# Performance work log

Measured on AMD Instinct MI355X. Metric: run time of the kernel, lower is better.

## Reference

```python
import jax, jax.numpy as jnp
import numpy as np

SAMPLING_FACTOR = 5


def setup_inputs() -> dict:
    key = jax.random.key(0)
    kq, kk, kv, ki = jax.random.split(key, 4)
    B, L, D = 32, 2048, 64
    return {
        "query_states": jax.random.normal(kq, (B, L, D), dtype=jnp.float32),
        "key_states": jax.random.normal(kk, (B, L, D), dtype=jnp.float32),
        "value_states": jax.random.normal(kv, (B, L, D), dtype=jnp.float32),
        "index_sample": jax.random.randint(ki, (L,), 0, L, dtype=jnp.int32),
    }


def reference(query_states, key_states, value_states, index_sample):
    B, L_Q, d_k = query_states.shape
    L_K = key_states.shape[1]
    log_L_K = int(np.ceil(np.log1p(L_K)))
    log_L_Q = int(np.ceil(np.log1p(L_Q)))
    U_part = min(SAMPLING_FACTOR * L_Q * log_L_K, L_K)
    u = min(SAMPLING_FACTOR * log_L_Q, L_Q)

    # random key sampling (indices supplied deterministically)
    idx = index_sample[:U_part]                       # [U_part]
    K_sample = jnp.take(key_states, idx, axis=1)      # [B, U_part, d]

    # sparsity measurement M(q) = max_k q.k - mean (original divides by L_K)
    Q_K_sample = jnp.einsum("bqd,bkd->bqk", query_states, K_sample)  # [B, L_Q, U_part]
    M = jnp.max(Q_K_sample, axis=-1) - jnp.sum(Q_K_sample, axis=-1) / jnp.float32(L_K)

    # top-u query selection
    _, M_top = jax.lax.top_k(M, u)                    # [B, u]
    Q_reduce = jnp.take_along_axis(query_states, M_top[..., None], axis=1)  # [B, u, d]

    # reduced attention
    attn_scores = jnp.einsum("bud,bkd->buk", Q_reduce, key_states) / jnp.sqrt(jnp.float32(d_k))
    attn_probs = jax.nn.softmax(attn_scores, axis=-1)
    attn_output = jnp.einsum("buk,bkd->bud", attn_probs, value_states)
    return attn_output, attn_scores
```

## Files before the change

### kernel.cpp

```cpp
#include <hip/hip_runtime.h>
#include <math.h>

#define BB 32
#define LL 2048
#define DD 64
#define UU 40
#define CC 64
#define FSEG 16
#define PSTR 42
#define NEG_BIG (-3.0e38f)

typedef __attribute__((ext_vector_type(8))) short short8;
typedef __attribute__((ext_vector_type(4))) float f32x4;
typedef unsigned long long ull;
typedef unsigned int uint;
typedef unsigned short ushort_t;

__device__ __forceinline__ unsigned short f2bf(float f) {
  uint u = __float_as_uint(f);
  u += 0x7FFFu + ((u >> 16) & 1u);
  return (unsigned short)(u >> 16);
}
__device__ __forceinline__ uint fsort(float f) {
  uint u = __float_as_uint(f);
  return (u & 0x80000000u) ? ~u : (u | 0x80000000u);
}
__device__ __forceinline__ ull shfl_xor_u64(ull x, int m) {
  uint lo = (uint)x, hi = (uint)(x >> 32);
  lo = __shfl_xor(lo, m);
  hi = __shfl_xor(hi, m);
  return ((ull)hi << 32) | lo;
}
__device__ __forceinline__ int4 pack_bf16x8(float4 a, float4 c4) {
  int4 o;
  o.x = (int)(f2bf(a.x) | ((uint)f2bf(a.y) << 16));
  o.y = (int)(f2bf(a.z) | ((uint)f2bf(a.w) << 16));
  o.z = (int)(f2bf(c4.x) | ((uint)f2bf(c4.y) << 16));
  o.w = (int)(f2bf(c4.z) | ((uint)f2bf(c4.w) << 16));
  return o;
}

__global__ __launch_bounds__(256) void prep_ksum_kernel(const float* __restrict__ K,
                                                        const int* __restrict__ idx,
                                                        ushort_t* __restrict__ Kg,
                                                        float* __restrict__ Kpart) {
  int p = blockIdx.x, b = blockIdx.y, t = threadIdx.x;
  int g = t & 7;
  float4 sa = {0.f, 0.f, 0.f, 0.f}, sb = {0.f, 0.f, 0.f, 0.f};
#pragma unroll
  for (int it = 0; it < 4; ++it) {
    int r = p * 128 + it * 32 + (t >> 3);
    int gk = idx[r];
    const float* src = K + ((size_t)b * LL + gk) * DD + g * 8;
    float4 a = *(const float4*)src;
    float4 c4 = *(const float4*)(src + 4);
    sa.x += a.x; sa.y += a.y; sa.z += a.z; sa.w += a.w;
    sb.x += c4.x; sb.y += c4.y; sb.z += c4.z; sb.w += c4.w;
    *(int4*)(Kg + ((size_t)b * LL + r) * DD + g * 8) = pack_bf16x8(a, c4);
  }
  __shared__ float red[32][64];
  int rt = t >> 3;
  *(float4*)&red[rt][g * 8] = sa;
  *(float4*)&red[rt][g * 8 + 4] = sb;
  __syncthreads();
  if (t < 64) {
    float s = 0.f;
#pragma unroll
    for (int r = 0; r < 32; ++r) s += red[r][t];
    Kpart[(b * 16 + p) * 64 + t] = s;
  }
}

__global__ __launch_bounds__(256) void mfma_m_kernel(const float* __restrict__ Q,
                                                     const ushort_t* __restrict__ Kg,
                                                     const float* __restrict__ Kpart,
                                                     float* __restrict__ Mb) {
  __shared__ __align__(16) ushort_t Qs[128 * 64];
  __shared__ __align__(16) ushort_t Ks[128 * 64];
  __shared__ float Mmax[2][128];
  __shared__ float KsumS[64];

  int b = blockIdx.y, q0 = blockIdx.x * 128;
  int t = threadIdx.x;
  int w = t >> 6, L = t & 63;

  if (t < 64) {
    float s = 0.f;
#pragma unroll
    for (int p = 0; p < 16; ++p) s += Kpart[(b * 16 + p) * 64 + t];
    KsumS[t] = s;
  }

  {
    int g = t & 7;
#pragma unroll
    for (int it = 0; it < 4; ++it) {
      int r = it * 32 + (t >> 3);
      const float* src = Q + ((size_t)b * LL + q0 + r) * DD + g * 8;
      float4 a = *(const float4*)src;
      float4 c4 = *(const float4*)(src + 4);
      *(int4*)&Qs[r * 64 + 8 * (g ^ (r & 7))] = pack_bf16x8(a, c4);
    }
  }

  f32x4 mx[4];
#pragma unroll
  for (int i = 0; i < 4; ++i) mx[i] = (f32x4){NEG_BIG, NEG_BIG, NEG_BIG, NEG_BIG};

  const int waveQ = 64 * (w & 1);
  const int waveK = 64 * (w >> 1);
  const int lm = L & 15;
  const int lq = L >> 4;

  for (int c = 0; c < LL / 128; ++c) {
    __syncthreads();
    {
      int g = t & 7;
#pragma unroll
      for (int it = 0; it < 4; ++it) {
        int r = it * 32 + (t >> 3);
        int4 v = *(const int4*)(Kg + ((size_t)b * LL + c * 128 + r) * DD + g * 8);
        *(int4*)&Ks[r * 64 + 8 * (g ^ (r & 7))] = v;
      }
    }
    __syncthreads();

    f32x4 acc[4][4];
#pragma unroll
    for (int i = 0; i < 4; ++i)
#pragma unroll
      for (int j = 0; j < 4; ++j) acc[i][j] = (f32x4){0.f, 0.f, 0.f, 0.f};

#pragma unroll
    for (int s = 0; s < 2; ++s) {
      int g = 4 * s + lq;
      short8 A[4];
#pragma unroll
      for (int qt = 0; qt < 4; ++qt) {
        int r = waveQ + 16 * qt + lm;
        A[qt] = *(const short8*)&Qs[r * 64 + 8 * (g ^ (r & 7))];
      }
#pragma unroll
      for (int kt = 0; kt < 4; ++kt) {
        int rB = waveK + 16 * kt + lm;
        short8 Bf = *(const short8*)&Ks[rB * 64 + 8 * (g ^ (rB & 7))];
#pragma unroll
        for (int qt = 0; qt < 4; ++qt) {
          acc[qt][kt] = __builtin_amdgcn_mfma_f32_16x16x32_bf16(A[qt], Bf, acc[qt][kt], 0, 0, 0);
        }
      }
    }
#pragma unroll
    for (int qt = 0; qt < 4; ++qt)
#pragma unroll
      for (int kt = 0; kt < 4; ++kt) {
#pragma unroll
        for (int r4 = 0; r4 < 4; ++r4) mx[qt][r4] = fmaxf(mx[qt][r4], acc[qt][kt][r4]);
      }
  }

#pragma unroll
  for (int qt = 0; qt < 4; ++qt) {
#pragma unroll
    for (int r4 = 0; r4 < 4; ++r4) {
      float v = mx[qt][r4];
      v = fmaxf(v, __shfl_xor(v, 1));
      v = fmaxf(v, __shfl_xor(v, 2));
      v = fmaxf(v, __shfl_xor(v, 4));
      v = fmaxf(v, __shfl_xor(v, 8));
      mx[qt][r4] = v;
    }
  }
  if (lm < 4) {
    int qt = lm;
#pragma unroll
    for (int r4 = 0; r4 < 4; ++r4) {
      Mmax[w >> 1][waveQ + 16 * qt + 4 * lq + r4] = mx[qt][r4];
    }
  }
  __syncthreads();

  if (t < 128) {
    float m = fmaxf(Mmax[0][t], Mmax[1][t]);
    const float4* Qr = (const float4*)(Q + ((size_t)b * LL + q0 + t) * DD);
    float s = 0.f;
#pragma unroll
    for (int i = 0; i < 16; ++i) {
      float4 qv = Qr[i];
      s += qv.x * KsumS[4 * i] + qv.y * KsumS[4 * i + 1] + qv.z * KsumS[4 * i + 2] +
           qv.w * KsumS[4 * i + 3];
    }
    Mb[b * LL + q0 + t] = m - s * (1.0f / (float)LL);
  }
}

__global__ __launch_bounds__(256) void cand_kernel(const float* __restrict__ Mb,
                                                   int* __restrict__ cand) {
  int b = blockIdx.x, t = threadIdx.x;
  int w = t >> 6;
  float v[8];
#pragma unroll
  for (int i = 0; i < 8; ++i) v[i] = Mb[b * LL + t + 256 * i];
  __shared__ ull warr[4];
  __shared__ ull winls;
  for (int round = 0; round < CC; ++round) {
    float bv = v[0];
    int bi = 0;
#pragma unroll
    for (int i = 1; i < 8; ++i)
      if (v[i] > bv) { bv = v[i]; bi = i; }
    ull key = ((ull)fsort(bv) << 32) | (ull)(uint)(t + 256 * bi);
#pragma unroll
    for (int m = 1; m < 64; m <<= 1) {
      ull o = shfl_xor_u64(key, m);
      if (o > key) key = o;
    }
    if ((t & 63) == 0) warr[w] = key;
    __syncthreads();
    if (t == 0) {
      ull k = warr[0];
#pragma unroll
      for (int i = 1; i < 4; ++i)
        if (warr[i] > k) k = warr[i];
      winls = k;
      cand[b * CC + round] = (int)(k & 0xFFFFFFFFull);
    }
    __syncthreads();
    int wj = (int)(winls & 0xFFFFFFFFull);
    if (t == (wj & 255)) v[wj >> 8] = NEG_BIG;
  }
}

__global__ __launch_bounds__(256) void rescue_kernel(const float* __restrict__ Q,
                                                     const float* __restrict__ K,
                                                     const int* __restrict__ idx,
                                                     const int* __restrict__ cand,
                                                     float* __restrict__ Mpart) {
  __shared__ float Qc[64][68];
  __shared__ float Kt[128][68];
  __shared__ float red[64][33];
  __shared__ int cidx[CC];
  int seg = blockIdx.x, b = blockIdx.y, t = threadIdx.x;

  if (t < CC) cidx[t] = cand[b * CC + t];
  __syncthreads();
  for (int li = t; li < 64 * 16; li += 256) {
    int row = li >> 4, g4 = li & 15;
    *(float4*)&Qc[row][4 * g4] =
        *(const float4*)(Q + ((size_t)b * LL + cidx[row]) * DD + 4 * g4);
  }
  for (int li = t; li < 128 * 16; li += 256) {
    int row = li >> 4, g4 = li & 15;
    int gk = idx[seg * 128 + row];
    *(float4*)&Kt[row][4 * g4] =
        *(const float4*)(K + ((size_t)b * LL + gk) * DD + 4 * g4);
  }
  __syncthreads();

  int tx = t & 7;
  int ty = t >> 3;
  float acc[8][4];
#pragma unroll
  for (int i = 0; i < 8; ++i)
#pragma unroll
    for (int j = 0; j < 4; ++j) acc[i][j] = 0.f;

#pragma unroll 4
  for (int dd = 0; dd < 64; dd += 4) {
    float4 qf[8];
#pragma unroll
    for (int i = 0; i < 8; ++i) qf[i] = *(const float4*)&Qc[tx + 8 * i][dd];
    float4 kf[4];
#pragma unroll
    for (int j = 0; j < 4; ++j) kf[j] = *(const float4*)&Kt[ty + 32 * j][dd];
#pragma unroll
    for (int i = 0; i < 8; ++i)
#pragma unroll
      for (int j = 0; j < 4; ++j) {
        float d = acc[i][j];
        d = fmaf(qf[i].x, kf[j].x, d);
        d = fmaf(qf[i].y, kf[j].y, d);
        d = fmaf(qf[i].z, kf[j].z, d);
        d = fmaf(qf[i].w, kf[j].w, d);
        acc[i][j] = d;
      }
  }

#pragma unroll
  for (int i = 0; i < 8; ++i) {
    float m = fmaxf(fmaxf(acc[i][0], acc[i][1]), fmaxf(acc[i][2], acc[i][3]));
    red[tx + 8 * i][ty] = m;
  }
  __syncthreads();
  if (t < CC) {
    float m = red[t][0];
#pragma unroll
    for (int tt = 1; tt < 32; ++tt) m = fmaxf(m, red[t][tt]);
    Mpart[((size_t)b * CC + t) * FSEG + seg] = m;
  }
}

__global__ __launch_bounds__(64) void select_kernel(const float* __restrict__ Q,
                                                    const float* __restrict__ Kpart,
                                                    const int* __restrict__ cand,
                                                    const float* __restrict__ Mpart,
                                                    int* __restrict__ topi) {
  int b = blockIdx.x, t = threadIdx.x;
  __shared__ float KsumS[64];
  __shared__ ull keys[CC];
  {
    float s = 0.f;
#pragma unroll
    for (int p = 0; p < 16; ++p) s += Kpart[(b * 16 + p) * 64 + t];
    KsumS[t] = s;
  }
  __syncthreads();
  int ci = cand[b * CC + t];
  float m = NEG_BIG;
#pragma unroll
  for (int s = 0; s < FSEG; ++s) m = fmaxf(m, Mpart[((size_t)b * CC + t) * FSEG + s]);
  const float4* Qr = (const float4*)(Q + ((size_t)b * LL + ci) * DD);
  float s = 0.f;
#pragma unroll
  for (int i = 0; i < 16; ++i) {
    float4 qv = Qr[i];
    s += qv.x * KsumS[4 * i] + qv.y * KsumS[4 * i + 1] + qv.z * KsumS[4 * i + 2] +
         qv.w * KsumS[4 * i + 3];
  }
  float Mf = m - s * (1.0f / (float)LL);
  ull key = ((ull)fsort(Mf) << 32) | (ull)(uint)(2047 - ci);
  keys[t] = key;
  __syncthreads();
  int rank = 0;
#pragma unroll 8
  for (int j = 0; j < CC; ++j) rank += (keys[j] > key) ? 1 : 0;
  if (rank < UU) topi[b * UU + rank] = ci;
}

__global__ __launch_bounds__(256, 2) void fused_epilogue_kernel(
    const float* __restrict__ Q, const float* __restrict__ K,
    const float* __restrict__ V, const int* __restrict__ topi,
    float* __restrict__ scores, float* __restrict__ Opart,
    float* __restrict__ lpart) {
  int seg = blockIdx.x, b = blockIdx.y, t = threadIdx.x;
  __shared__ int cidx[UU];
  __shared__ float Qc[UU][DD];
  __shared__ float pT[128 * PSTR];
  __shared__ float lw[4][20];

  if (t < UU) cidx[t] = topi[b * UU + t];
  __syncthreads();
  for (int li = t; li < UU * 16; li += 256) {
    int u = li >> 4, g4 = li & 15;
    *(float4*)&Qc[u][4 * g4] =
        *(const float4*)(Q + ((size_t)b * LL + cidx[u]) * DD + 4 * g4);
  }
  __syncthreads();

  int kl = t & 127, uh = t >> 7, w = t >> 6;
  int k = seg * 128 + kl;
  float4 kr[16];
  const float4* Krow = (const float4*)(K + ((size_t)b * LL + k) * DD);
#pragma unroll
  for (int i = 0; i < 16; ++i) kr[i] = Krow[i];

  float p[20];
#pragma unroll 4
  for (int j = 0; j < 20; ++j) {
    int u = uh * 20 + j;
    const float4* qp = (const float4*)&Qc[u][0];
    float s = 0.f;
#pragma unroll
    for (int i = 0; i < 16; ++i) {
      float4 qv = qp[i];
      s += qv.x * kr[i].x + qv.y * kr[i].y + qv.z * kr[i].z + qv.w * kr[i].w;
    }
    s *= 0.125f;
    scores[((size_t)(b * UU + u)) * LL + k] = s;
    p[j] = __expf(s);
  }

#pragma unroll
  for (int j = 0; j < 20; ++j) {
    float ls = p[j];
#pragma unroll
    for (int off = 32; off > 0; off >>= 1) ls += __shfl_xor(ls, off);
    if ((t & 63) == 0) lw[w][j] = ls;
  }
#pragma unroll
  for (int j = 0; j < 20; j += 2) {
    *(float2*)&pT[kl * PSTR + uh * 20 + j] = make_float2(p[j], p[j + 1]);
  }
  __syncthreads();
  if (t < UU) {
    int u = t;
    float ls = (u < 20) ? (lw[0][u] + lw[1][u]) : (lw[2][u - 20] + lw[3][u - 20]);
    lpart[(size_t)(b * FSEG + seg) * UU + u] = ls;
  }

  int d4 = t & 15, c = t >> 4;
  int ug = c & 7, kq = c >> 3;
  int u0 = ug * 5;
  float4 acc[5];
#pragma unroll
  for (int j = 0; j < 5; ++j) acc[j] = (float4){0.f, 0.f, 0.f, 0.f};
  const float* Vb = V + ((size_t)b * LL + seg * 128 + kq * 64) * DD;
  for (int kk = 0; kk < 64; ++kk) {
    float4 v4 = *(const float4*)(Vb + (size_t)kk * DD + 4 * d4);
    const float* prow = &pT[(kq * 64 + kk) * PSTR + u0];
#pragma unroll
    for (int j = 0; j < 5; ++j) {
      float pj = prow[j];
      acc[j].x += pj * v4.x; acc[j].y += pj * v4.y;
      acc[j].z += pj * v4.z; acc[j].w += pj * v4.w;
    }
  }
  __syncthreads();
  float* red = pT;
#pragma unroll
  for (int j = 0; j < 5; ++j)
    *(float4*)&red[(kq * 40 + u0 + j) * 64 + 4 * d4] = acc[j];
  __syncthreads();
  for (int li = t; li < UU * DD; li += 256) {
    int u = li >> 6, d = li & 63;
    float s = red[u * 64 + d] + red[(40 + u) * 64 + d];
    Opart[((size_t)(b * FSEG + seg) * UU + u) * DD + d] = s;
  }
}

__global__ __launch_bounds__(256) void combine_kernel(const float* __restrict__ Opart,
                                                      const float* __restrict__ lpart,
                                                      float* __restrict__ out) {
  int b = blockIdx.x, t = threadIdx.x;
  __shared__ float Linv[UU];
  if (t < UU) {
    float Lsum = 0.f;
#pragma unroll
    for (int s = 0; s < FSEG; ++s) Lsum += lpart[(size_t)(b * FSEG + s) * UU + t];
    Linv[t] = 1.0f / Lsum;
  }
  __syncthreads();
  for (int li = t; li < UU * DD; li += 256) {
    int u = li >> 6, d = li & 63;
    float O = 0.f;
#pragma unroll
    for (int s = 0; s < FSEG; ++s)
      O += Opart[((size_t)(b * FSEG + s) * UU + u) * DD + d];
    out[((size_t)b * UU + u) * DD + d] = O * Linv[u];
  }
}

__global__ __launch_bounds__(256) void ksum_kernel(const float* __restrict__ K,
                                                   const int* __restrict__ idx,
                                                   float* __restrict__ Kpart) {
  int p = blockIdx.x, b = blockIdx.y, tid = threadIdx.x;
  int d = tid & 63, c = tid >> 6;
  const float* Kb = K + (size_t)b * LL * DD;
  float acc = 0.f;
  int j0 = p * 128 + c * 32;
#pragma unroll 4
  for (int t = 0; t < 32; ++t) acc += Kb[(size_t)idx[j0 + t] * DD + d];
  __shared__ float red[256];
  red[tid] = acc;
  __syncthreads();
  if (c == 0) Kpart[(b * 16 + p) * 64 + d] = red[d] + red[64 + d] + red[128 + d] + red[192 + d];
}

__global__ __launch_bounds__(256) void m_kernel(const float* __restrict__ Q,
                                                const float* __restrict__ K,
                                                const int* __restrict__ idx,
                                                const float* __restrict__ Kpart,
                                                float* __restrict__ M) {
  __shared__ float Qs[128][68];
  __shared__ float Ks[128][68];
  __shared__ float KsumS[64];
  __shared__ float red[128][17];
  int b = blockIdx.y, q0 = blockIdx.x * 128, tid = threadIdx.x;
  int tx = tid & 15, ty = tid >> 4;
  if (tid < 64) {
    float s = 0.f;
#pragma unroll
    for (int p = 0; p < 16; ++p) s += Kpart[(b * 16 + p) * 64 + tid];
    KsumS[tid] = s;
  }
#pragma unroll
  for (int it = 0; it < 8; ++it) {
    int li = it * 256 + tid;
    int q = li >> 4, dd = (li & 15) << 2;
    *(float4*)&Qs[q][dd] = *(const float4*)(Q + ((size_t)b * LL + q0 + q) * DD + dd);
  }
  float mx[8];
#pragma unroll
  for (int i = 0; i < 8; ++i) mx[i] = NEG_BIG;
  for (int c = 0; c < LL / 128; ++c) {
    __syncthreads();
#pragma unroll
    for (int it = 0; it < 8; ++it) {
      int li = it * 256 + tid;
      int kk = li >> 4, dd = (li & 15) << 2;
      int gk = idx[c * 128 + kk];
      *(float4*)&Ks[kk][dd] = *(const float4*)(K + ((size_t)b * LL + gk) * DD + dd);
    }
    __syncthreads();
    float acc[8][8];
#pragma unroll
    for (int i = 0; i < 8; ++i)
#pragma unroll
      for (int j = 0; j < 8; ++j) acc[i][j] = 0.f;
#pragma unroll 2
    for (int dd = 0; dd < 64; dd += 4) {
      float4 qf[8];
#pragma unroll
      for (int i = 0; i < 8; ++i) qf[i] = *(const float4*)&Qs[tx + 16 * i][dd];
#pragma unroll
      for (int j = 0; j < 8; ++j) {
        float4 kf = *(const float4*)&Ks[ty + 16 * j][dd];
#pragma unroll
        for (int i = 0; i < 8; ++i)
          acc[i][j] += qf[i].x * kf.x + qf[i].y * kf.y + qf[i].z * kf.z + qf[i].w * kf.w;
      }
    }
#pragma unroll
    for (int i = 0; i < 8; ++i) {
      float m01 = fmaxf(fmaxf(acc[i][0], acc[i][1]), fmaxf(acc[i][2], acc[i][3]));
      float m23 = fmaxf(fmaxf(acc[i][4], acc[i][5]), fmaxf(acc[i][6], acc[i][7]));
      mx[i] = fmaxf(mx[i], fmaxf(m01, m23));
    }
  }
  __syncthreads();
#pragma unroll
  for (int i = 0; i < 8; ++i) red[tx + 16 * i][ty] = mx[i];
  __syncthreads();
  if (tid < 128) {
    float m = red[tid][0];
#pragma unroll
    for (int tt = 1; tt < 16; ++tt) m = fmaxf(m, red[tid][tt]);
    float s = 0.f;
#pragma unroll 16
    for (int d = 0; d < 64; ++d) s += Qs[tid][d] * KsumS[d];
    M[b * LL + q0 + tid] = m - s * (1.0f / (float)LL);
  }
}

__global__ __launch_bounds__(256) void topk_kernel(const float* __restrict__ M,
                                                   int* __restrict__ topi) {
  int b = blockIdx.x, tid = threadIdx.x;
  __shared__ float mv[LL];
  __shared__ float wv[4];
  __shared__ int wi[4];
  for (int j = tid; j < LL; j += 256) mv[j] = M[b * LL + j];
  __syncthreads();
  for (int t = 0; t < UU; ++t) {
    float bv = NEG_BIG;
    int bi = 0x7fffffff;
    for (int j = tid; j < LL; j += 256) {
      float v = mv[j];
      if (v > bv) { bv = v; bi = j; }
    }
#pragma unroll
    for (int off = 32; off > 0; off >>= 1) {
      float ov = __shfl_down(bv, off);
      int oi = __shfl_down(bi, off);
      if (ov > bv || (ov == bv && oi < bi)) { bv = ov; bi = oi; }
    }
    if ((tid & 63) == 0) { wv[tid >> 6] = bv; wi[tid >> 6] = bi; }
    __syncthreads();
    if (tid == 0) {
#pragma unroll
      for (int w = 1; w < 4; ++w)
        if (wv[w] > bv || (wv[w] == bv && wi[w] < bi)) { bv = wv[w]; bi = wi[w]; }
      topi[b * UU + t] = bi;
      mv[bi] = NEG_BIG;
    }
    __syncthreads();
  }
}

__global__ __launch_bounds__(256) void scores_kernel(const float* __restrict__ Q,
                                                     const float* __restrict__ K,
                                                     const int* __restrict__ topi,
                                                     float* __restrict__ scores) {
  int b = blockIdx.y;
  int k = blockIdx.x * 256 + threadIdx.x;
  __shared__ float Qr[UU][DD];
  for (int li = threadIdx.x; li < UU * DD; li += 256) {
    int u = li >> 6, d = li & 63;
    Qr[u][d] = Q[((size_t)b * LL + topi[b * UU + u]) * DD + d];
  }
  __syncthreads();
  float4 kr[16];
  const float4* Krow = (const float4*)(K + ((size_t)b * LL + k) * DD);
#pragma unroll
  for (int i = 0; i < 16; ++i) kr[i] = Krow[i];
  for (int u = 0; u < UU; ++u) {
    float s = 0.f;
#pragma unroll
    for (int i = 0; i < 16; ++i) {
      float4 qv = *(const float4*)&Qr[u][i << 2];
      s += qv.x * kr[i].x + qv.y * kr[i].y + qv.z * kr[i].z + qv.w * kr[i].w;
    }
    scores[((size_t)(b * UU + u)) * LL + k] = s * 0.125f;
  }
}

__global__ __launch_bounds__(256) void softmax_pv_kernel(const float* __restrict__ scores,
                                                         const float* __restrict__ V,
                                                         float* __restrict__ out) {
  int b = blockIdx.y;
  int u0 = blockIdx.x * 4;
  int tid = threadIdx.x;
  __shared__ float p[4][LL];
  __shared__ float wred[4];
  __shared__ float inv_s[4];
  __shared__ float r2[256];
#pragma unroll
  for (int uu = 0; uu < 4; ++uu) {
    const float* srow = scores + ((size_t)(b * UU + u0 + uu)) * LL;
    float m = NEG_BIG;
    for (int j = tid; j < LL; j += 256) m = fmaxf(m, srow[j]);
#pragma unroll
    for (int off = 32; off > 0; off >>= 1) m = fmaxf(m, __shfl_down(m, off));
    if ((tid & 63) == 0) wred[tid >> 6] = m;
    __syncthreads();
    float smax = fmaxf(fmaxf(wred[0], wred[1]), fmaxf(wred[2], wred[3]));
    __syncthreads();
    float ls = 0.f;
    for (int j = tid; j < LL; j += 256) {
      float e = __expf(srow[j] - smax);
      p[uu][j] = e;
      ls += e;
    }
#pragma unroll
    for (int off = 32; off > 0; off >>= 1) ls += __shfl_down(ls, off);
    if ((tid & 63) == 0) wred[tid >> 6] = ls;
    __syncthreads();
    if (tid == 0) inv_s[uu] = 1.0f / (wred[0] + wred[1] + wred[2] + wred[3]);
    __syncthreads();
  }
  int d = tid & 63, c = tid >> 6;
  float acc[4] = {0.f, 0.f, 0.f, 0.f};
  const float* Vb = V + (size_t)b * LL * DD;
  int k0 = c * (LL / 4), k1 = k0 + (LL / 4);
  for (int k = k0; k < k1; ++k) {
    float v = Vb[(size_t)k * DD + d];
#pragma unroll
    for (int uu = 0; uu < 4; ++uu) acc[uu] += p[uu][k] * v;
  }
#pragma unroll
  for (int uu = 0; uu < 4; ++uu) {
    r2[tid] = acc[uu];
    __syncthreads();
    if (c == 0) {
      out[((size_t)(b * UU) + u0 + uu) * DD + d] =
          (r2[d] + r2[64 + d] + r2[128 + d] + r2[192 + d]) * inv_s[uu];
    }
    __syncthreads();
  }
}

extern "C" void kernel_launch(void* const* d_in, const int* in_sizes, int n_in,
                              void* d_out, int out_size, void* d_ws, size_t ws_size,
                              hipStream_t stream) {
  (void)in_sizes; (void)n_in; (void)out_size;
  const float* Q = (const float*)d_in[0];
  const float* K = (const float*)d_in[1];
  const float* V = (const float*)d_in[2];
  const int* idx = (const int*)d_in[3];

  float* out = (float*)d_out;
  float* scores = out + (size_t)BB * UU * DD;

  const size_t kg_off = 0;
  const size_t kpart_off = kg_off + (size_t)BB * LL * DD * sizeof(ushort_t);
  const size_t mb_off = kpart_off + (size_t)BB * 16 * DD * sizeof(float);
  const size_t mpart_off = mb_off + (size_t)BB * LL * sizeof(float);
  const size_t cand_off = mpart_off + (size_t)BB * CC * FSEG * sizeof(float);
  const size_t topi_off = cand_off + (size_t)BB * CC * sizeof(int);
  const size_t need = topi_off + (size_t)BB * UU * sizeof(int);

  char* ws = (char*)d_ws;
  if (ws_size >= need) {
    ushort_t* Kg = (ushort_t*)(ws + kg_off);
    float* Kpart = (float*)(ws + kpart_off);
    float* Mb = (float*)(ws + mb_off);
    float* Mpart = (float*)(ws + mpart_off);
    int* cand = (int*)(ws + cand_off);
    int* topi = (int*)(ws + topi_off);
    float* Opart = (float*)(ws + kg_off);
    float* lpart = Opart + (size_t)BB * FSEG * UU * DD;

    prep_ksum_kernel<<<dim3(16, BB), 256, 0, stream>>>(K, idx, Kg, Kpart);
    mfma_m_kernel<<<dim3(LL / 128, BB), 256, 0, stream>>>(Q, Kg, Kpart, Mb);
    cand_kernel<<<BB, 256, 0, stream>>>(Mb, cand);
    rescue_kernel<<<dim3(FSEG, BB), 256, 0, stream>>>(Q, K, idx, cand, Mpart);
    select_kernel<<<BB, 64, 0, stream>>>(Q, Kpart, cand, Mpart, topi);
    fused_epilogue_kernel<<<dim3(FSEG, BB), 256, 0, stream>>>(Q, K, V, topi, scores,
                                                              Opart, lpart);
    combine_kernel<<<BB, 256, 0, stream>>>(Opart, lpart, out);
  } else {
    size_t need2 =
        (size_t)(BB * LL + BB * 16 * DD) * sizeof(float) + (size_t)(BB * UU) * sizeof(int);
    float* M;
    float* Kpart;
    int* topi;
    if (ws_size >= need2) {
      M = (float*)d_ws;
      Kpart = M + BB * LL;
      topi = (int*)(Kpart + BB * 16 * DD);
    } else {
      M = scores;
      Kpart = scores + BB * LL;
      topi = (int*)out;
    }
    ksum_kernel<<<dim3(16, BB), 256, 0, stream>>>(K, idx, Kpart);
    m_kernel<<<dim3(LL / 128, BB), 256, 0, stream>>>(Q, K, idx, Kpart, M);
    topk_kernel<<<BB, 256, 0, stream>>>(M, topi);
    scores_kernel<<<dim3(LL / 256, BB), 256, 0, stream>>>(Q, K, topi, scores);
    softmax_pv_kernel<<<dim3(UU / 4, BB), 256, 0, stream>>>(scores, V, out);
  }
}
```

Baseline: 220.0 us.

## Split sampled-key range across two blocks and prefetch K tiles into registers

```diff
diff --git a/kernel.cpp b/kernel.cpp
--- a/kernel.cpp
+++ b/kernel.cpp
@@ -74,28 +74,33 @@
 __global__ __launch_bounds__(256) void mfma_m_kernel(const float* __restrict__ Q,
                                                      const ushort_t* __restrict__ Kg,
                                                      const float* __restrict__ Kpart,
-                                                     float* __restrict__ Mb) {
+                                                     float* __restrict__ Mhalf,
+                                                     float* __restrict__ Mmean) {
   __shared__ __align__(16) ushort_t Qs[128 * 64];
   __shared__ __align__(16) ushort_t Ks[128 * 64];
   __shared__ float Mmax[2][128];
   __shared__ float KsumS[64];
 
-  int b = blockIdx.y, q0 = blockIdx.x * 128;
+  int bx = blockIdx.x;
+  int b = blockIdx.y;
+  int qt = bx >> 1, h = bx & 1;
+  int q0 = qt * 128;
   int t = threadIdx.x;
   int w = t >> 6, L = t & 63;
 
-  if (t < 64) {
+  if (h == 0 && t < 64) {
     float s = 0.f;
 #pragma unroll
     for (int p = 0; p < 16; ++p) s += Kpart[(b * 16 + p) * 64 + t];
     KsumS[t] = s;
   }
 
+  int g = t & 7;
+  int rbase = t >> 3;
   {
-    int g = t & 7;
 #pragma unroll
     for (int it = 0; it < 4; ++it) {
-      int r = it * 32 + (t >> 3);
+      int r = it * 32 + rbase;
       const float* src = Q + ((size_t)b * LL + q0 + r) * DD + g * 8;
       float4 a = *(const float4*)src;
       float4 c4 = *(const float4*)(src + 4);
@@ -112,18 +117,26 @@
   const int lm = L & 15;
   const int lq = L >> 4;
 
-  for (int c = 0; c < LL / 128; ++c) {
-    __syncthreads();
-    {
-      int g = t & 7;
-#pragma unroll
-      for (int it = 0; it < 4; ++it) {
-        int r = it * 32 + (t >> 3);
-        int4 v = *(const int4*)(Kg + ((size_t)b * LL + c * 128 + r) * DD + g * 8);
-        *(int4*)&Ks[r * 64 + 8 * (g ^ (r & 7))] = v;
-      }
-    }
-    __syncthreads();
+  const ushort_t* KgH = Kg + ((size_t)b * LL + h * 1024) * DD;
+
+  int4 pre[4];
+#pragma unroll
+  for (int it = 0; it < 4; ++it)
+    pre[it] = *(const int4*)(KgH + (size_t)(it * 32 + rbase) * DD + g * 8);
+
+  for (int c = 0; c < 8; ++c) {
+    __syncthreads();
+#pragma unroll
+    for (int it = 0; it < 4; ++it) {
+      int r = it * 32 + rbase;
+      *(int4*)&Ks[r * 64 + 8 * (g ^ (r & 7))] = pre[it];
+    }
+    __syncthreads();
+    if (c < 7) {
+#pragma unroll
+      for (int it = 0; it < 4; ++it)
+        pre[it] = *(const int4*)(KgH + (size_t)((c + 1) * 128 + it * 32 + rbase) * DD + g * 8);
+    }
 
     f32x4 acc[4][4];
 #pragma unroll
@@ -133,74 +146,82 @@
 
 #pragma unroll
     for (int s = 0; s < 2; ++s) {
-      int g = 4 * s + lq;
+      int gg = 4 * s + lq;
       short8 A[4];
 #pragma unroll
-      for (int qt = 0; qt < 4; ++qt) {
-        int r = waveQ + 16 * qt + lm;
-        A[qt] = *(const short8*)&Qs[r * 64 + 8 * (g ^ (r & 7))];
+      for (int qt2 = 0; qt2 < 4; ++qt2) {
+        int r = waveQ + 16 * qt2 + lm;
+        A[qt2] = *(const short8*)&Qs[r * 64 + 8 * (gg ^ (r & 7))];
       }
 #pragma unroll
       for (int kt = 0; kt < 4; ++kt) {
         int rB = waveK + 16 * kt + lm;
-        short8 Bf = *(const short8*)&Ks[rB * 64 + 8 * (g ^ (rB & 7))];
-#pragma unroll
-        for (int qt = 0; qt < 4; ++qt) {
-          acc[qt][kt] = __builtin_amdgcn_mfma_f32_16x16x32_bf16(A[qt], Bf, acc[qt][kt], 0, 0, 0);
+        short8 Bf = *(const short8*)&Ks[rB * 64 + 8 * (gg ^ (rB & 7))];
+#pragma unroll
+        for (int qt2 = 0; qt2 < 4; ++qt2) {
+          acc[qt2][kt] = __builtin_amdgcn_mfma_f32_16x16x32_bf16(A[qt2], Bf, acc[qt2][kt], 0, 0, 0);
         }
       }
     }
 #pragma unroll
-    for (int qt = 0; qt < 4; ++qt)
+    for (int qt2 = 0; qt2 < 4; ++qt2)
 #pragma unroll
       for (int kt = 0; kt < 4; ++kt) {
 #pragma unroll
-        for (int r4 = 0; r4 < 4; ++r4) mx[qt][r4] = fmaxf(mx[qt][r4], acc[qt][kt][r4]);
+        for (int r4 = 0; r4 < 4; ++r4) mx[qt2][r4] = fmaxf(mx[qt2][r4], acc[qt2][kt][r4]);
       }
   }
 
 #pragma unroll
-  for (int qt = 0; qt < 4; ++qt) {
+  for (int qt2 = 0; qt2 < 4; ++qt2) {
 #pragma unroll
     for (int r4 = 0; r4 < 4; ++r4) {
-      float v = mx[qt][r4];
+      float v = mx[qt2][r4];
       v = fmaxf(v, __shfl_xor(v, 1));
       v = fmaxf(v, __shfl_xor(v, 2));
       v = fmaxf(v, __shfl_xor(v, 4));
       v = fmaxf(v, __shfl_xor(v, 8));
-      mx[qt][r4] = v;
+      mx[qt2][r4] = v;
     }
   }
   if (lm < 4) {
-    int qt = lm;
+    int qt2 = lm;
 #pragma unroll
     for (int r4 = 0; r4 < 4; ++r4) {
-      Mmax[w >> 1][waveQ + 16 * qt + 4 * lq + r4] = mx[qt][r4];
+      Mmax[w >> 1][waveQ + 16 * qt2 + 4 * lq + r4] = mx[qt2][r4];
     }
   }
   __syncthreads();
 
   if (t < 128) {
     float m = fmaxf(Mmax[0][t], Mmax[1][t]);
-    const float4* Qr = (const float4*)(Q + ((size_t)b * LL + q0 + t) * DD);
-    float s = 0.f;
-#pragma unroll
-    for (int i = 0; i < 16; ++i) {
-      float4 qv = Qr[i];
-      s += qv.x * KsumS[4 * i] + qv.y * KsumS[4 * i + 1] + qv.z * KsumS[4 * i + 2] +
-           qv.w * KsumS[4 * i + 3];
-    }
-    Mb[b * LL + q0 + t] = m - s * (1.0f / (float)LL);
-  }
-}
-
-__global__ __launch_bounds__(256) void cand_kernel(const float* __restrict__ Mb,
+    Mhalf[((size_t)b * 2 + h) * LL + q0 + t] = m;
+    if (h == 0) {
+      const float4* Qr = (const float4*)(Q + ((size_t)b * LL + q0 + t) * DD);
+      float s = 0.f;
+#pragma unroll
+      for (int i = 0; i < 16; ++i) {
+        float4 qv = Qr[i];
+        s += qv.x * KsumS[4 * i] + qv.y * KsumS[4 * i + 1] + qv.z * KsumS[4 * i + 2] +
+             qv.w * KsumS[4 * i + 3];
+      }
+      Mmean[b * LL + q0 + t] = s * (1.0f / (float)LL);
+    }
+  }
+}
+
+__global__ __launch_bounds__(256) void cand_kernel(const float* __restrict__ Mhalf,
+                                                   const float* __restrict__ Mmean,
                                                    int* __restrict__ cand) {
   int b = blockIdx.x, t = threadIdx.x;
   int w = t >> 6;
   float v[8];
 #pragma unroll
-  for (int i = 0; i < 8; ++i) v[i] = Mb[b * LL + t + 256 * i];
+  for (int i = 0; i < 8; ++i) {
+    int q = t + 256 * i;
+    float m = fmaxf(Mhalf[((size_t)b * 2) * LL + q], Mhalf[((size_t)b * 2 + 1) * LL + q]);
+    v[i] = m - Mmean[b * LL + q];
+  }
   __shared__ ull warr[4];
   __shared__ ull winls;
   for (int round = 0; round < CC; ++round) {
@@ -672,8 +693,9 @@
 
   const size_t kg_off = 0;
   const size_t kpart_off = kg_off + (size_t)BB * LL * DD * sizeof(ushort_t);
-  const size_t mb_off = kpart_off + (size_t)BB * 16 * DD * sizeof(float);
-  const size_t mpart_off = mb_off + (size_t)BB * LL * sizeof(float);
+  const size_t mhalf_off = kpart_off + (size_t)BB * 16 * DD * sizeof(float);
+  const size_t mmean_off = mhalf_off + (size_t)BB * 2 * LL * sizeof(float);
+  const size_t mpart_off = mmean_off + (size_t)BB * LL * sizeof(float);
   const size_t cand_off = mpart_off + (size_t)BB * CC * FSEG * sizeof(float);
   const size_t topi_off = cand_off + (size_t)BB * CC * sizeof(int);
   const size_t need = topi_off + (size_t)BB * UU * sizeof(int);
@@ -682,7 +704,8 @@
   if (ws_size >= need) {
     ushort_t* Kg = (ushort_t*)(ws + kg_off);
     float* Kpart = (float*)(ws + kpart_off);
-    float* Mb = (float*)(ws + mb_off);
+    float* Mhalf = (float*)(ws + mhalf_off);
+    float* Mmean = (float*)(ws + mmean_off);
     float* Mpart = (float*)(ws + mpart_off);
     int* cand = (int*)(ws + cand_off);
     int* topi = (int*)(ws + topi_off);
@@ -690,8 +713,8 @@
     float* lpart = Opart + (size_t)BB * FSEG * UU * DD;
 
     prep_ksum_kernel<<<dim3(16, BB), 256, 0, stream>>>(K, idx, Kg, Kpart);
-    mfma_m_kernel<<<dim3(LL / 128, BB), 256, 0, stream>>>(Q, Kg, Kpart, Mb);
-    cand_kernel<<<BB, 256, 0, stream>>>(Mb, cand);
+    mfma_m_kernel<<<dim3(32, BB), 256, 0, stream>>>(Q, Kg, Kpart, Mhalf, Mmean);
+    cand_kernel<<<BB, 256, 0, stream>>>(Mhalf, Mmean, cand);
     rescue_kernel<<<dim3(FSEG, BB), 256, 0, stream>>>(Q, K, idx, cand, Mpart);
     select_kernel<<<BB, 64, 0, stream>>>(Q, Kpart, cand, Mpart, topi);
     fused_epilogue_kernel<<<dim3(FSEG, BB), 256, 0, stream>>>(Q, K, V, topi, scores,
```

Result: slower. 246.0 us (+11.8%).

## Double-buffer sampled-K tiles with async global-to-LDS loads and pre-swizzled layout

Applied to the files above, without the earlier changes.

```diff
diff --git a/kernel.cpp b/kernel.cpp
--- a/kernel.cpp
+++ b/kernel.cpp
@@ -39,6 +39,10 @@
   o.w = (int)(f2bf(c4.z) | ((uint)f2bf(c4.w) << 16));
   return o;
 }
+__device__ __forceinline__ void async_copy16(const void* g, void* l) {
+  __builtin_amdgcn_global_load_lds((const __attribute__((address_space(1))) void*)g,
+                                   (__attribute__((address_space(3))) void*)l, 16, 0, 0);
+}
 
 __global__ __launch_bounds__(256) void prep_ksum_kernel(const float* __restrict__ K,
                                                         const int* __restrict__ idx,
@@ -56,7 +60,7 @@
     float4 c4 = *(const float4*)(src + 4);
     sa.x += a.x; sa.y += a.y; sa.z += a.z; sa.w += a.w;
     sb.x += c4.x; sb.y += c4.y; sb.z += c4.z; sb.w += c4.w;
-    *(int4*)(Kg + ((size_t)b * LL + r) * DD + g * 8) = pack_bf16x8(a, c4);
+    *(int4*)(Kg + ((size_t)b * LL + r) * DD + 8 * (g ^ (r & 7))) = pack_bf16x8(a, c4);
   }
   __shared__ float red[32][64];
   int rt = t >> 3;
@@ -76,13 +80,22 @@
                                                      const float* __restrict__ Kpart,
                                                      float* __restrict__ Mb) {
   __shared__ __align__(16) ushort_t Qs[128 * 64];
-  __shared__ __align__(16) ushort_t Ks[128 * 64];
+  __shared__ __align__(16) ushort_t Ks[2][128 * 64];
   __shared__ float Mmax[2][128];
   __shared__ float KsumS[64];
 
   int b = blockIdx.y, q0 = blockIdx.x * 128;
   int t = threadIdx.x;
   int w = t >> 6, L = t & 63;
+
+  const ushort_t* KgB = Kg + (size_t)b * LL * DD;
+
+#pragma unroll
+  for (int i = 0; i < 4; ++i) {
+    const ushort_t* gp =
+        KgB + (size_t)(w * 32 + i * 8 + (L >> 3)) * DD + (L & 7) * 8;
+    async_copy16(gp, &Ks[0][(w * 32 + i * 8) * 64]);
+  }
 
   if (t < 64) {
     float s = 0.f;
@@ -102,6 +115,7 @@
       *(int4*)&Qs[r * 64 + 8 * (g ^ (r & 7))] = pack_bf16x8(a, c4);
     }
   }
+  __syncthreads();
 
   f32x4 mx[4];
 #pragma unroll
@@ -113,17 +127,16 @@
   const int lq = L >> 4;
 
   for (int c = 0; c < LL / 128; ++c) {
-    __syncthreads();
-    {
-      int g = t & 7;
-#pragma unroll
-      for (int it = 0; it < 4; ++it) {
-        int r = it * 32 + (t >> 3);
-        int4 v = *(const int4*)(Kg + ((size_t)b * LL + c * 128 + r) * DD + g * 8);
-        *(int4*)&Ks[r * 64 + 8 * (g ^ (r & 7))] = v;
+    int cur = c & 1;
+    if (c < LL / 128 - 1) {
+      int nxt = cur ^ 1;
+#pragma unroll
+      for (int i = 0; i < 4; ++i) {
+        const ushort_t* gp =
+            KgB + (size_t)((c + 1) * 128 + w * 32 + i * 8 + (L >> 3)) * DD + (L & 7) * 8;
+        async_copy16(gp, &Ks[nxt][(w * 32 + i * 8) * 64]);
       }
     }
-    __syncthreads();
 
     f32x4 acc[4][4];
 #pragma unroll
@@ -143,7 +156,7 @@
 #pragma unroll
       for (int kt = 0; kt < 4; ++kt) {
         int rB = waveK + 16 * kt + lm;
-        short8 Bf = *(const short8*)&Ks[rB * 64 + 8 * (g ^ (rB & 7))];
+        short8 Bf = *(const short8*)&Ks[cur][rB * 64 + 8 * (g ^ (rB & 7))];
 #pragma unroll
         for (int qt = 0; qt < 4; ++qt) {
           acc[qt][kt] = __builtin_amdgcn_mfma_f32_16x16x32_bf16(A[qt], Bf, acc[qt][kt], 0, 0, 0);
@@ -157,6 +170,7 @@
 #pragma unroll
         for (int r4 = 0; r4 < 4; ++r4) mx[qt][r4] = fmaxf(mx[qt][r4], acc[qt][kt][r4]);
       }
+    __syncthreads();
   }
 
 #pragma unroll
```

Result: faster. 203.9 us (-7.3%).
